# Kernel optimization log

Hardware: AMD Instinct MI355X
Metric: run time of the kernel (lower is better)

The kernel has to match this reference:

```python
import jax, jax.numpy as jnp
import numpy as np

BN_EPS = 1e-5


def setup_inputs() -> dict:
    key = jax.random.key(0)
    k1, k2, k3 = jax.random.split(key, 3)
    B, C, R, N = 512, 256, 8, 81
    x = jax.random.normal(k1, (B, C, 9, 9), dtype=jnp.float32)
    adj = jax.random.uniform(k2, (B, R, N, N), dtype=jnp.float32)
    # xavier-uniform-like init for per-relation weights
    limit = float(np.sqrt(6.0 / (C + C)))
    weight = jax.random.uniform(k3, (R, C, C), dtype=jnp.float32, minval=-limit, maxval=limit)
    gamma = jnp.ones((C,), dtype=jnp.float32)
    beta = jnp.zeros((C,), dtype=jnp.float32)
    return {"x": x, "adj": adj, "weight": weight, "gamma": gamma, "beta": beta}


def reference(x, adj, weight, gamma, beta):
    B, C = x.shape[0], x.shape[1]
    N = 81
    # (B, C, 9, 9) -> (B, N, C) node features
    h = x.reshape(B, C, N).transpose(0, 2, 1)
    # per-relation message passing: msg_r = adj_r @ h, then msg_r @ W_r, summed over r
    msg = jnp.einsum('brnm,bmc->brnc', adj, h)          # (B, R, N, C)
    out_h = jnp.einsum('brnc,rcd->bnd', msg, weight)    # (B, N, C)
    out = out_h.transpose(0, 2, 1).reshape(B, C, 9, 9)
    pre = out + x
    # BatchNorm2d (training mode): biased batch stats over (N, H, W) per channel
    mean = jnp.mean(pre, axis=(0, 2, 3), keepdims=True)
    var = jnp.mean(jnp.square(pre - mean), axis=(0, 2, 3), keepdims=True)
    norm = (pre - mean) * jax.lax.rsqrt(var + BN_EPS)
    bn = norm * gamma[None, :, None, None] + beta[None, :, None, None]
    return jax.nn.relu(bn)
```

## Files before the change

kernel.cpp:

```cpp
#include <hip/hip_runtime.h>


#define B_SZ 512
#define C_SZ 256
#define R_SZ 8
#define N_SZ 81
#define TH 512

typedef short bf16x8 __attribute__((ext_vector_type(8)));
typedef float f32x4 __attribute__((ext_vector_type(4)));

__device__ __forceinline__ unsigned short f2bf(float f) {
    union { float f; unsigned u; } v; v.f = f;
    unsigned r = v.u + 0x7FFFu + ((v.u >> 16) & 1u);
    return (unsigned short)(r >> 16);
}

__device__ __forceinline__ unsigned long long pack4bf(f32x4 v) {
    unsigned long long r;
    r  = (unsigned long long)f2bf(v[0]);
    r |= (unsigned long long)f2bf(v[1]) << 16;
    r |= (unsigned long long)f2bf(v[2]) << 32;
    r |= (unsigned long long)f2bf(v[3]) << 48;
    return r;
}

#define ADJ_OFF 0
#define MSG_OFF 8448
#define SMEM_SZ (8448 + 48 * 512 + 32)

__device__ __forceinline__ int msg_addr(int n, int cbyte) {
    int s = (n ^ (n >> 3)) & 7;
    return MSG_OFF + n * 512 + (cbyte ^ (s << 4));
}

__global__ void prep_wt(const float* __restrict__ w, unsigned short* __restrict__ wt) {
    int i = blockIdx.x * blockDim.x + threadIdx.x;
    if (i >= R_SZ * C_SZ * C_SZ) return;
    int r = i >> 16;
    int d = (i >> 8) & 255;
    int c = i & 255;
    wt[i] = f2bf(w[(r * C_SZ + c) * C_SZ + d]);
}

__launch_bounds__(TH, 4)
__global__ void rgcn_main(const float* __restrict__ x,
                          const float* __restrict__ adj,
                          const unsigned short* __restrict__ wt,
                          float* __restrict__ out,
                          float* __restrict__ psum) {
    __shared__ __align__(16) unsigned char smem[SMEM_SZ];
    unsigned short* adjs = (unsigned short*)(smem + ADJ_OFF);

    const int bid  = blockIdx.x;
    const int xcd  = bid & 7;
    const int slot = bid >> 3;
    const int b    = xcd * 64 + (slot >> 1);
    const int half = slot & 1;
    const int n0   = half * 48;
    const int nvalid = half ? 33 : 48;
    const int cnt  = nvalid * N_SZ;

    const int tid  = threadIdx.x;
    const int lane = tid & 63;
    const int wave = tid >> 6;
    const int lr   = lane & 15;
    const int lk   = lane >> 4;
    const int cb   = wave * 32;

    const float* xb   = x + (size_t)b * C_SZ * N_SZ;
    const float* adjb = adj + ((size_t)b * R_SZ * N_SZ + n0) * N_SZ;

    bf16x8 hfr[3][2];
#pragma unroll
    for (int kk = 0; kk < 3; ++kk) {
#pragma unroll
        for (int jc = 0; jc < 2; ++jc) {
            int c = cb + jc * 16 + lr;
            const float* src = xb + c * N_SZ;
#pragma unroll
            for (int e = 0; e < 8; ++e) {
                int m = kk * 32 + lk * 8 + e;
                hfr[kk][jc][e] = (m < N_SZ) ? (short)f2bf(src[m]) : (short)0;
            }
        }
    }

    for (int i = tid; i < (48 * 88) / 2; i += TH) ((unsigned*)adjs)[i] = 0;

    float pf[8];
#pragma unroll
    for (int u = 0; u < 8; ++u) {
        int i2 = tid + u * TH;
        pf[u] = (i2 < cnt) ? adjb[i2] : 0.f;
    }
    __syncthreads();
#pragma unroll
    for (int u = 0; u < 8; ++u) {
        int i2 = tid + u * TH;
        if (i2 < cnt) {
            int n = i2 / N_SZ, m = i2 - n * N_SZ;
            adjs[n * 88 + m] = f2bf(pf[u]);
        }
    }
    __syncthreads();

    const f32x4 vzero = {0.f, 0.f, 0.f, 0.f};
    f32x4 acc[2][3];
#pragma unroll
    for (int jd = 0; jd < 2; ++jd)
#pragma unroll
        for (int jn = 0; jn < 3; ++jn) acc[jd][jn] = vzero;

    for (int r = 0; r < R_SZ; ++r) {
        if (r < R_SZ - 1) {
            const float* an = adjb + (r + 1) * (N_SZ * N_SZ);
#pragma unroll
            for (int u = 0; u < 8; ++u) {
                int i2 = tid + u * TH;
                pf[u] = (i2 < cnt) ? an[i2] : 0.f;
            }
        }

        f32x4 macc[2][3];
#pragma unroll
        for (int jc = 0; jc < 2; ++jc)
#pragma unroll
            for (int jn = 0; jn < 3; ++jn) macc[jc][jn] = vzero;

#pragma unroll
        for (int kk = 0; kk < 3; ++kk) {
            bf16x8 bfr[3];
#pragma unroll
            for (int jn = 0; jn < 3; ++jn)
                bfr[jn] = *(const bf16x8*)&adjs[(jn * 16 + lr) * 88 + kk * 32 + lk * 8];
#pragma unroll
            for (int jc = 0; jc < 2; ++jc)
#pragma unroll
                for (int jn = 0; jn < 3; ++jn)
                    macc[jc][jn] = __builtin_amdgcn_mfma_f32_16x16x32_bf16(hfr[kk][jc], bfr[jn], macc[jc][jn], 0, 0, 0);
        }

        const unsigned short* wr = wt + r * (C_SZ * C_SZ);
        bf16x8 wA[2][2], wB[2][2];
#pragma unroll
        for (int dk = 0; dk < 2; ++dk)
#pragma unroll
            for (int jd = 0; jd < 2; ++jd)
                wA[dk][jd] = *(const bf16x8*)&wr[(cb + jd * 16 + lr) * 256 + dk * 32 + lk * 8];

        __syncthreads();

#pragma unroll
        for (int jc = 0; jc < 2; ++jc) {
#pragma unroll
            for (int jn = 0; jn < 3; ++jn) {
                int n = jn * 16 + lr;
                int cbyte = (cb + jc * 16 + lk * 4) * 2;
                *(unsigned long long*)(smem + msg_addr(n, cbyte)) = pack4bf(macc[jc][jn]);
            }
        }
        if (r < R_SZ - 1) {
#pragma unroll
            for (int u = 0; u < 8; ++u) {
                int i2 = tid + u * TH;
                if (i2 < cnt) {
                    int n = i2 / N_SZ, m = i2 - n * N_SZ;
                    adjs[n * 88 + m] = f2bf(pf[u]);
                }
            }
        }
        __syncthreads();

        auto do2 = [&](bf16x8 (&wc)[2][2], bf16x8 (&wn)[2][2], int kk0, bool load) {
            if (load) {
#pragma unroll
                for (int dk = 0; dk < 2; ++dk)
#pragma unroll
                    for (int jd = 0; jd < 2; ++jd)
                        wn[dk][jd] = *(const bf16x8*)&wr[(cb + jd * 16 + lr) * 256 + (kk0 + 2 + dk) * 32 + lk * 8];
            }
#pragma unroll
            for (int dk = 0; dk < 2; ++dk) {
                int kk = kk0 + dk;
                bf16x8 bfr[3];
#pragma unroll
                for (int jn = 0; jn < 3; ++jn)
                    bfr[jn] = *(const bf16x8*)(smem + msg_addr(jn * 16 + lr, kk * 64 + lk * 16));
#pragma unroll
                for (int jd = 0; jd < 2; ++jd)
#pragma unroll
                    for (int jn = 0; jn < 3; ++jn)
                        acc[jd][jn] = __builtin_amdgcn_mfma_f32_16x16x32_bf16(wc[dk][jd], bfr[jn], acc[jd][jn], 0, 0, 0);
            }
        };
        do2(wA, wB, 0, true);
        do2(wB, wA, 2, true);
        do2(wA, wB, 4, true);
        do2(wB, wA, 6, false);
    }

    float* outb = out + (size_t)b * C_SZ * N_SZ;
    const int bh = b * 2 + half;
#pragma unroll
    for (int jd = 0; jd < 2; ++jd) {
        float s1[4] = {0.f, 0.f, 0.f, 0.f};
        float s2[4] = {0.f, 0.f, 0.f, 0.f};
#pragma unroll
        for (int jn = 0; jn < 3; ++jn) {
            int nloc = jn * 16 + lr;
            bool ok = nloc < nvalid;
            int n = n0 + nloc;
#pragma unroll
            for (int q = 0; q < 4; ++q) {
                int d = cb + jd * 16 + lk * 4 + q;
                if (ok) {
                    float pre = acc[jd][jn][q] + xb[d * N_SZ + n];
                    outb[d * N_SZ + n] = pre;
                    s1[q] += pre;
                    s2[q] += pre * pre;
                }
            }
        }
#pragma unroll
        for (int q = 0; q < 4; ++q) {
#pragma unroll
            for (int msk = 8; msk > 0; msk >>= 1) {
                s1[q] += __shfl_xor(s1[q], msk);
                s2[q] += __shfl_xor(s2[q], msk);
            }
        }
        if (lr == 0) {
#pragma unroll
            for (int q = 0; q < 4; ++q) {
                int d = cb + jd * 16 + lk * 4 + q;
                psum[(size_t)d * 1024 + bh] = s1[q];
                psum[(size_t)C_SZ * 1024 + (size_t)d * 1024 + bh] = s2[q];
            }
        }
    }
}

__global__ void bn_stats(const float* __restrict__ psum,
                         const float* __restrict__ gamma, const float* __restrict__ beta,
                         float* __restrict__ mr) {
    int c = blockIdx.x;
    int t = threadIdx.x;
    float a = 0.f, s = 0.f;
    for (int k = t; k < 1024; k += 64) {
        a += psum[(size_t)c * 1024 + k];
        s += psum[(size_t)C_SZ * 1024 + (size_t)c * 1024 + k];
    }
#pragma unroll
    for (int off = 32; off > 0; off >>= 1) {
        a += __shfl_down(a, off);
        s += __shfl_down(s, off);
    }
    if (t == 0) {
        const float inv = 1.0f / (float)(B_SZ * N_SZ);
        float mean = a * inv;
        float var = s * inv - mean * mean;
        float rstd = rsqrtf(var + 1e-5f);
        float scale = rstd * gamma[c];
        mr[c] = scale;
        mr[256 + c] = beta[c] - mean * scale;
    }
}

__global__ void bn_apply(float* __restrict__ out, const float* __restrict__ mr) {
    const int total4 = (B_SZ * C_SZ * N_SZ) / 4;
    f32x4* o4 = (f32x4*)out;
    for (int i = blockIdx.x * blockDim.x + threadIdx.x; i < total4;
         i += gridDim.x * blockDim.x) {
        f32x4 v = o4[i];
        int e0 = i * 4;
#pragma unroll
        for (int k = 0; k < 4; ++k) {
            int c = ((e0 + k) / N_SZ) & 255;
            float t = v[k] * mr[c] + mr[256 + c];
            v[k] = t > 0.f ? t : 0.f;
        }
        o4[i] = v;
    }
}

extern "C" void kernel_launch(void* const* d_in, const int* in_sizes, int n_in,
                              void* d_out, int out_size, void* d_ws, size_t ws_size,
                              hipStream_t stream) {
    const float* x     = (const float*)d_in[0];
    const float* adj   = (const float*)d_in[1];
    const float* w     = (const float*)d_in[2];
    const float* gamma = (const float*)d_in[3];
    const float* beta  = (const float*)d_in[4];
    float* out = (float*)d_out;

    unsigned short* wt = (unsigned short*)d_ws;
    char* p = (char*)d_ws + (size_t)R_SZ * C_SZ * C_SZ * 2;
    float* psum = (float*)p;
    float* mr = (float*)(p + (size_t)2 * 1024 * C_SZ * 4);

    prep_wt<<<(R_SZ * C_SZ * C_SZ + 255) / 256, 256, 0, stream>>>(w, wt);
    rgcn_main<<<1024, TH, 0, stream>>>(x, adj, wt, out, psum);
    bn_stats<<<C_SZ, 64, 0, stream>>>(psum, gamma, beta, mr);
    bn_apply<<<2048, 256, 0, stream>>>(out, mr);
}
```

Measured before the change: 235.5 us.

## Double-buffer adjacency and message LDS tiles to drop one barrier per relation

Splits the adjacency and message shared-memory regions into two ping-pong buffers, so each relation iteration needs a single barrier instead of two. The global prefetch of the adjacency tile now runs two relations ahead. Weight fragments use a four-slot rotating register window, loaded three k-steps ahead. The cost is double the LDS footprint (about 66KB per block) and higher register pressure, which can lower occupancy under launch_bounds(512,4).

```diff
diff --git a/kernel.cpp b/kernel.cpp
--- a/kernel.cpp
+++ b/kernel.cpp
@@ -25,13 +25,15 @@
     return r;
 }
 
-#define ADJ_OFF 0
-#define MSG_OFF 8448
-#define SMEM_SZ (8448 + 48 * 512 + 32)
-
-__device__ __forceinline__ int msg_addr(int n, int cbyte) {
+#define ADJ_OFF  0
+#define MSG_OFF  16896
+#define SMEM_SZ  (16896 + 49152 + 32)
+
+__device__ __forceinline__ int adj_base(int buf) { return ADJ_OFF + buf * 8448; }
+
+__device__ __forceinline__ int msg_addr(int buf, int n, int cbyte) {
     int s = (n ^ (n >> 3)) & 7;
-    return MSG_OFF + n * 512 + (cbyte ^ (s << 4));
+    return MSG_OFF + buf * 24576 + n * 512 + (cbyte ^ (s << 4));
 }
 
 __global__ void prep_wt(const float* __restrict__ w, unsigned short* __restrict__ wt) {
@@ -50,7 +52,6 @@
                           float* __restrict__ out,
                           float* __restrict__ psum) {
     __shared__ __align__(16) unsigned char smem[SMEM_SZ];
-    unsigned short* adjs = (unsigned short*)(smem + ADJ_OFF);
 
     const int bid  = blockIdx.x;
     const int xcd  = bid & 7;
@@ -86,7 +87,7 @@
         }
     }
 
-    for (int i = tid; i < (48 * 88) / 2; i += TH) ((unsigned*)adjs)[i] = 0;
+    for (int i = tid; i < 16896 / 4; i += TH) ((unsigned*)smem)[i] = 0;
 
     float pf[8];
 #pragma unroll
@@ -95,13 +96,21 @@
         pf[u] = (i2 < cnt) ? adjb[i2] : 0.f;
     }
     __syncthreads();
+    {
+        unsigned short* a0 = (unsigned short*)(smem + adj_base(0));
+#pragma unroll
+        for (int u = 0; u < 8; ++u) {
+            int i2 = tid + u * TH;
+            if (i2 < cnt) {
+                int n = i2 / N_SZ, m = i2 - n * N_SZ;
+                a0[n * 88 + m] = f2bf(pf[u]);
+            }
+        }
+    }
 #pragma unroll
     for (int u = 0; u < 8; ++u) {
         int i2 = tid + u * TH;
-        if (i2 < cnt) {
-            int n = i2 / N_SZ, m = i2 - n * N_SZ;
-            adjs[n * 88 + m] = f2bf(pf[u]);
-        }
+        pf[u] = (i2 < cnt) ? adjb[1 * (N_SZ * N_SZ) + i2] : 0.f;
     }
     __syncthreads();
 
@@ -112,14 +121,19 @@
 #pragma unroll
         for (int jn = 0; jn < 3; ++jn) acc[jd][jn] = vzero;
 
+#pragma unroll 1
     for (int r = 0; r < R_SZ; ++r) {
-        if (r < R_SZ - 1) {
-            const float* an = adjb + (r + 1) * (N_SZ * N_SZ);
-#pragma unroll
-            for (int u = 0; u < 8; ++u) {
-                int i2 = tid + u * TH;
-                pf[u] = (i2 < cnt) ? an[i2] : 0.f;
-            }
+        const int cur = r & 1;
+        const unsigned short* adjc = (const unsigned short*)(smem + adj_base(cur));
+        const unsigned short* wr   = wt + r * (C_SZ * C_SZ);
+
+        bf16x8 w0[2], w1[2], w2[2], w3[2];
+#pragma unroll
+        for (int jd = 0; jd < 2; ++jd) {
+            const unsigned short* wrow = wr + (cb + jd * 16 + lr) * 256 + lk * 8;
+            w0[jd] = *(const bf16x8*)&wrow[0 * 32];
+            w1[jd] = *(const bf16x8*)&wrow[1 * 32];
+            w2[jd] = *(const bf16x8*)&wrow[2 * 32];
         }
 
         f32x4 macc[2][3];
@@ -133,23 +147,13 @@
             bf16x8 bfr[3];
 #pragma unroll
             for (int jn = 0; jn < 3; ++jn)
-                bfr[jn] = *(const bf16x8*)&adjs[(jn * 16 + lr) * 88 + kk * 32 + lk * 8];
+                bfr[jn] = *(const bf16x8*)&adjc[(jn * 16 + lr) * 88 + kk * 32 + lk * 8];
 #pragma unroll
             for (int jc = 0; jc < 2; ++jc)
 #pragma unroll
                 for (int jn = 0; jn < 3; ++jn)
                     macc[jc][jn] = __builtin_amdgcn_mfma_f32_16x16x32_bf16(hfr[kk][jc], bfr[jn], macc[jc][jn], 0, 0, 0);
         }
-
-        const unsigned short* wr = wt + r * (C_SZ * C_SZ);
-        bf16x8 wA[2][2], wB[2][2];
-#pragma unroll
-        for (int dk = 0; dk < 2; ++dk)
-#pragma unroll
-            for (int jd = 0; jd < 2; ++jd)
-                wA[dk][jd] = *(const bf16x8*)&wr[(cb + jd * 16 + lr) * 256 + dk * 32 + lk * 8];
-
-        __syncthreads();
 
 #pragma unroll
         for (int jc = 0; jc < 2; ++jc) {
@@ -157,47 +161,52 @@
             for (int jn = 0; jn < 3; ++jn) {
                 int n = jn * 16 + lr;
                 int cbyte = (cb + jc * 16 + lk * 4) * 2;
-                *(unsigned long long*)(smem + msg_addr(n, cbyte)) = pack4bf(macc[jc][jn]);
-            }
-        }
+                *(unsigned long long*)(smem + msg_addr(cur, n, cbyte)) = pack4bf(macc[jc][jn]);
+            }
+        }
+
         if (r < R_SZ - 1) {
+            unsigned short* an = (unsigned short*)(smem + adj_base(cur ^ 1));
 #pragma unroll
             for (int u = 0; u < 8; ++u) {
                 int i2 = tid + u * TH;
                 if (i2 < cnt) {
                     int n = i2 / N_SZ, m = i2 - n * N_SZ;
-                    adjs[n * 88 + m] = f2bf(pf[u]);
+                    an[n * 88 + m] = f2bf(pf[u]);
                 }
             }
-        }
+            if (r < R_SZ - 2) {
+                const float* src = adjb + (r + 2) * (N_SZ * N_SZ);
+#pragma unroll
+                for (int u = 0; u < 8; ++u) {
+                    int i2 = tid + u * TH;
+                    pf[u] = (i2 < cnt) ? src[i2] : 0.f;
+                }
+            }
+        }
+
         __syncthreads();
 
-        auto do2 = [&](bf16x8 (&wc)[2][2], bf16x8 (&wn)[2][2], int kk0, bool load) {
-            if (load) {
-#pragma unroll
-                for (int dk = 0; dk < 2; ++dk)
-#pragma unroll
-                    for (int jd = 0; jd < 2; ++jd)
-                        wn[dk][jd] = *(const bf16x8*)&wr[(cb + jd * 16 + lr) * 256 + (kk0 + 2 + dk) * 32 + lk * 8];
-            }
-#pragma unroll
-            for (int dk = 0; dk < 2; ++dk) {
-                int kk = kk0 + dk;
-                bf16x8 bfr[3];
+        bf16x8* wsets[4] = {w0, w1, w2, w3};
+#pragma unroll
+        for (int kk = 0; kk < 8; ++kk) {
+            if (kk + 3 < 8) {
+                bf16x8* wn = wsets[(kk + 3) & 3];
+#pragma unroll
+                for (int jd = 0; jd < 2; ++jd)
+                    wn[jd] = *(const bf16x8*)&wr[(cb + jd * 16 + lr) * 256 + (kk + 3) * 32 + lk * 8];
+            }
+            bf16x8* wc = wsets[kk & 3];
+            bf16x8 bfr[3];
+#pragma unroll
+            for (int jn = 0; jn < 3; ++jn)
+                bfr[jn] = *(const bf16x8*)(smem + msg_addr(cur, jn * 16 + lr, kk * 64 + lk * 16));
+#pragma unroll
+            for (int jd = 0; jd < 2; ++jd)
 #pragma unroll
                 for (int jn = 0; jn < 3; ++jn)
-                    bfr[jn] = *(const bf16x8*)(smem + msg_addr(jn * 16 + lr, kk * 64 + lk * 16));
-#pragma unroll
-                for (int jd = 0; jd < 2; ++jd)
-#pragma unroll
-                    for (int jn = 0; jn < 3; ++jn)
-                        acc[jd][jn] = __builtin_amdgcn_mfma_f32_16x16x32_bf16(wc[dk][jd], bfr[jn], acc[jd][jn], 0, 0, 0);
-            }
-        };
-        do2(wA, wB, 0, true);
-        do2(wB, wA, 2, true);
-        do2(wA, wB, 4, true);
-        do2(wB, wA, 6, false);
+                    acc[jd][jn] = __builtin_amdgcn_mfma_f32_16x16x32_bf16(wc[jd], bfr[jn], acc[jd][jn], 0, 0, 0);
+        }
     }
 
     float* outb = out + (size_t)b * C_SZ * N_SZ;
```

After: 400.6 us. 1.7x slower.
